# Kernel tuning notes

Hardware: AMD Instinct MI355X
Metric: run time of the kernel (lower is better)

Reference implementation:

```python
import jax, jax.numpy as jnp
import numpy as np

NUM_HEADS = 16
KEY_DIM = 64
EPS = 1e-6


def setup_inputs() -> dict:
    key = jax.random.key(0)
    k0, k1, k2, k3, k4 = jax.random.split(key, 5)
    B, S, E = 4, 4096, NUM_HEADS * KEY_DIM
    scale = 1.0 / np.sqrt(KEY_DIM)
    return {
        "query": jax.random.normal(k0, (B, S, E), dtype=jnp.float32),
        "Wq": jax.random.normal(k1, (NUM_HEADS, KEY_DIM, KEY_DIM), dtype=jnp.float32) * scale,
        "Wk": jax.random.normal(k2, (NUM_HEADS, KEY_DIM, KEY_DIM), dtype=jnp.float32) * scale,
        "Wv": jax.random.normal(k3, (NUM_HEADS, KEY_DIM, KEY_DIM), dtype=jnp.float32) * scale,
        "Wo": jax.random.normal(k4, (E, E), dtype=jnp.float32) * (1.0 / np.sqrt(E)),
    }


def reference(query, Wq, Wk, Wv, Wo):
    # Self-attention: key = value = query (per call() defaults).
    B, S, E = query.shape
    H, D = NUM_HEADS, KEY_DIM
    # split_heads: (B, S, E) -> (B, H, S, D)
    x = jnp.transpose(query.reshape(B, S, H, D), (0, 2, 1, 3))
    # Per-head linear projections (all heads batched in one einsum each).
    q = jnp.einsum("bhsd,hde->bhse", x, Wq)
    k = jnp.einsum("bhsd,hde->bhse", x, Wk)
    v = jnp.einsum("bhsd,hde->bhse", x, Wv)
    # Kernel feature map phi(x) = elu(x) + 1 (strictly positive).
    phi_q = jax.nn.elu(q) + 1.0
    phi_k = jax.nn.elu(k) + 1.0
    # Linear (non-causal) attention: O(S*D^2) instead of O(S^2*D).
    kv = jnp.einsum("bhsd,bhse->bhde", phi_k, v)        # (B,H,D,D)
    k_sum = jnp.sum(phi_k, axis=2)                       # (B,H,D)
    z = jnp.einsum("bhsd,bhd->bhs", phi_q, k_sum)        # (B,H,S)
    ctx = jnp.einsum("bhsd,bhde->bhse", phi_q, kv) / (z[..., None] + EPS)
    # combine_heads: (B,H,S,D) -> (B,S,E), then output projection (no bias).
    combined = jnp.transpose(ctx, (0, 2, 1, 3)).reshape(B, S, H * D)
    return combined @ Wo
```

## Files before the change

### kernel.cpp

```cpp
#include <hip/hip_runtime.h>
#include <stdint.h>

#define S_LEN 4096
#define NHEADS 16
#define DHEAD 64
#define EMB 1024
#define NBATCH 4
#define NBH (NBATCH * NHEADS)

typedef unsigned short u16t;
typedef __attribute__((ext_vector_type(8))) short short8;
typedef __attribute__((ext_vector_type(4))) float f32x4;

__device__ __forceinline__ u16t f2bf(float f) {
  unsigned int x = __float_as_uint(f);
  x += 0x7fffu + ((x >> 16) & 1u);
  return (u16t)(x >> 16);
}
__device__ __forceinline__ unsigned int pack2(float a, float b) {
  return (unsigned int)f2bf(a) | ((unsigned int)f2bf(b) << 16);
}
__device__ __forceinline__ float bf2f(u16t u) { return __uint_as_float(((unsigned int)u) << 16); }
__device__ __forceinline__ float phifn(float v) { return v > 0.f ? v + 1.f : __expf(v); }

__device__ __forceinline__ void stage_x_bf16(const float* __restrict__ xg,
                                             u16t* __restrict__ xs, int t) {
#pragma unroll
  for (int i = 0; i < 8; ++i) {
    int fi = i * 256 + t;
    int r = fi >> 4, c4 = fi & 15;
    float4 v = *(const float4*)(xg + (size_t)r * EMB + c4 * 4);
    uint2 p;
    p.x = pack2(v.x, v.y);
    p.y = pack2(v.z, v.w);
    *(uint2*)(&xs[r * 72 + c4 * 4]) = p;
  }
}

__device__ __forceinline__ void stage_w8k(const u16t* __restrict__ wg,
                                          u16t* __restrict__ lds, int t) {
#pragma unroll
  for (int c = 0; c < 2; ++c) {
    const u16t* src = wg + (size_t)(c * 256 + t) * 8;
    char* dst = (char*)lds + c * 4096 + ((t >> 6) << 10);
    __builtin_amdgcn_global_load_lds((const __attribute__((address_space(1))) unsigned int*)src,
                                     (__attribute__((address_space(3))) unsigned int*)dst,
                                     16, 0, 0);
  }
}

__global__ __launch_bounds__(256) void la_prep(const float* __restrict__ Wq,
                                               const float* __restrict__ Wk,
                                               const float* __restrict__ Wv,
                                               u16t* __restrict__ WqT,
                                               u16t* __restrict__ WkT,
                                               u16t* __restrict__ WvT) {
  __shared__ float tmp[64][65];
  int blk = blockIdx.x;
  int mat = blk >> 4, h = blk & 15;
  const float* src = (mat == 0 ? Wq : (mat == 1 ? Wk : Wv)) + (size_t)h * 4096;
  u16t* dst = (mat == 0 ? WqT : (mat == 1 ? WkT : WvT)) + (size_t)h * 4096;
  int t = threadIdx.x;
#pragma unroll
  for (int p = 0; p < 16; ++p) {
    int i = p * 256 + t;
    tmp[i >> 6][i & 63] = src[i];
  }
  __syncthreads();
#pragma unroll
  for (int p = 0; p < 16; ++p) {
    int i = p * 256 + t;
    int e = i >> 6, r = i & 63, o = r >> 3, j = r & 7;
    dst[i] = f2bf(tmp[((o ^ (e & 7)) << 3) + j][e]);
  }
}

__global__ __launch_bounds__(256) void la_wot(const float* __restrict__ Wo,
                                              u16t* __restrict__ WoT) {
  __shared__ float t[64][65];
  int n0 = blockIdx.x * 64, k0 = blockIdx.y * 64;
  int tx = threadIdx.x, ty = threadIdx.y;
  for (int r = ty; r < 64; r += 4) t[r][tx] = Wo[(size_t)(k0 + r) * EMB + n0 + tx];
  __syncthreads();
  for (int r = ty; r < 64; r += 4)
    WoT[(size_t)(n0 + r) * EMB + k0 + tx] = f2bf(t[tx][r]);
}

__global__ __launch_bounds__(256) void la_kvq3(const float* __restrict__ q,
                                               const u16t* __restrict__ WqT,
                                               const u16t* __restrict__ WkT,
                                               const u16t* __restrict__ WvT,
                                               u16t* __restrict__ phiq,
                                               float* __restrict__ kvpart,
                                               float* __restrict__ kspart) {
  __shared__ u16t xs[128 * 72];
  __shared__ u16t wq[4096];
  __shared__ u16t wk[4096];
  __shared__ u16t wv[4096];
  __shared__ u16t pkT[64 * 136];
  __shared__ u16t vT[64 * 136];
  int blk = blockIdx.x;
  int bh = blk >> 3, tile = blk & 7;
  int b = bh >> 4, h = bh & 15;
  int s0 = tile << 9;
  int t = threadIdx.x;
  int wave = t >> 6, lane = t & 63, l16 = lane & 15, g = lane >> 4;

  stage_w8k(WqT + (size_t)h * 4096, wq, t);
  stage_w8k(WkT + (size_t)h * 4096, wk, t);
  stage_w8k(WvT + (size_t)h * 4096, wv, t);

  f32x4 kacc[4];
#pragma unroll
  for (int n = 0; n < 4; ++n) kacc[n] = 0.f;
  float ksacc = 0.f;

  for (int c = 0; c < 4; ++c) {
    if (c) __syncthreads();
    stage_x_bf16(q + ((size_t)b * S_LEN + s0 + c * 128) * EMB + h * 64, xs, t);
    __syncthreads();

    f32x4 aQ[2][4], aK[2][4], aV[2][4];
#pragma unroll
    for (int m = 0; m < 2; ++m)
#pragma unroll
      for (int n = 0; n < 4; ++n) { aQ[m][n] = 0.f; aK[m][n] = 0.f; aV[m][n] = 0.f; }
    short8 af[2][2];
#pragma unroll
    for (int m = 0; m < 2; ++m)
#pragma unroll
      for (int kk = 0; kk < 2; ++kk)
        af[m][kk] = *(const short8*)(&xs[(wave * 32 + m * 16 + l16) * 72 + kk * 32 + g * 8]);
#pragma unroll
    for (int n = 0; n < 4; ++n) {
      int e = n * 16 + l16;
#pragma unroll
      for (int kk = 0; kk < 2; ++kk) {
        int op = (kk * 4 + g) ^ (l16 & 7);
        short8 bQ = *(const short8*)(&wq[e * 64 + op * 8]);
        short8 bK = *(const short8*)(&wk[e * 64 + op * 8]);
        short8 bV = *(const short8*)(&wv[e * 64 + op * 8]);
#pragma unroll
        for (int m = 0; m < 2; ++m) {
          aQ[m][n] = __builtin_amdgcn_mfma_f32_16x16x32_bf16(af[m][kk], bQ, aQ[m][n], 0, 0, 0);
          aK[m][n] = __builtin_amdgcn_mfma_f32_16x16x32_bf16(af[m][kk], bK, aK[m][n], 0, 0, 0);
          aV[m][n] = __builtin_amdgcn_mfma_f32_16x16x32_bf16(af[m][kk], bV, aV[m][n], 0, 0, 0);
        }
      }
    }
    __syncthreads();

#pragma unroll
    for (int m = 0; m < 2; ++m)
#pragma unroll
      for (int n = 0; n < 4; ++n) {
        int e = n * 16 + l16;
#pragma unroll
        for (int j = 0; j < 4; ++j) {
          int s = wave * 32 + m * 16 + g * 4 + j;
          xs[s * 72 + e] = f2bf(phifn(aQ[m][n][j]));
          pkT[e * 136 + s] = f2bf(phifn(aK[m][n][j]));
          vT[e * 136 + s] = f2bf(aV[m][n][j]);
        }
      }
    __syncthreads();

#pragma unroll
    for (int i = 0; i < 4; ++i) {
      int slot = i * 256 + t;
      int r = slot >> 3, cc = (slot & 7) * 8;
      *(uint4*)(phiq + ((size_t)bh * S_LEN + s0 + c * 128 + r) * 64 + cc) =
          *(const uint4*)(&xs[r * 72 + cc]);
    }
#pragma unroll
    for (int ks = 0; ks < 4; ++ks) {
      short8 pa = *(const short8*)(&pkT[(wave * 16 + l16) * 136 + ks * 32 + g * 8]);
#pragma unroll
      for (int n = 0; n < 4; ++n) {
        short8 vb = *(const short8*)(&vT[(n * 16 + l16) * 136 + ks * 32 + g * 8]);
        kacc[n] = __builtin_amdgcn_mfma_f32_16x16x32_bf16(pa, vb, kacc[n], 0, 0, 0);
      }
    }
    if (t < 64) {
#pragma unroll 8
      for (int s = 0; s < 128; ++s) ksacc += bf2f(pkT[t * 136 + s]);
    }
  }

  float* kp = kvpart + (size_t)blk * 4096;
#pragma unroll
  for (int n = 0; n < 4; ++n)
#pragma unroll
    for (int j = 0; j < 4; ++j)
      kp[(wave * 16 + g * 4 + j) * 64 + n * 16 + l16] = kacc[n][j];
  if (t < 64) kspart[(size_t)blk * 64 + t] = ksacc;
}

__global__ __launch_bounds__(256) void la_red3(const float* __restrict__ kvpart,
                                               const float* __restrict__ kspart,
                                               const u16t* __restrict__ WoT,
                                               float* __restrict__ ksum_g,
                                               u16t* __restrict__ W2T) {
  __shared__ float kvs[64][65];
  __shared__ u16t aT[256 * 72];
  int bh = blockIdx.x;
  int b = bh >> 4, h = bh & 15;
  int t = threadIdx.x, wave = t >> 6, lane = t & 63, l16 = lane & 15, g = lane >> 4;

  float acc[16];
#pragma unroll
  for (int i = 0; i < 16; ++i) acc[i] = 0.f;
  for (int p = 0; p < 8; ++p) {
    const float* base = kvpart + ((size_t)bh * 8 + p) * 4096;
#pragma unroll
    for (int i = 0; i < 16; ++i) acc[i] += base[i * 256 + t];
  }
#pragma unroll
  for (int i = 0; i < 16; ++i) {
    int idx = i * 256 + t;
    kvs[idx >> 6][idx & 63] = acc[i];
  }
  if (t < 64) {
    float a = 0.f;
    for (int p = 0; p < 8; ++p) a += kspart[((size_t)bh * 8 + p) * 64 + t];
    ksum_g[(size_t)bh * 64 + t] = a;
  }
  __syncthreads();

  short8 kvbf[4][2];
#pragma unroll
  for (int n = 0; n < 4; ++n)
#pragma unroll
    for (int kk = 0; kk < 2; ++kk) {
      u16t* pp = (u16t*)&kvbf[n][kk];
#pragma unroll
      for (int i = 0; i < 8; ++i) pp[i] = f2bf(kvs[n * 16 + l16][kk * 32 + g * 8 + i]);
    }

  for (int ec = 0; ec < 4; ++ec) {
    if (ec) __syncthreads();
#pragma unroll
    for (int p = 0; p < 8; ++p) {
      int slot = p * 256 + t;
      int r = slot >> 3, cc = (slot & 7) * 8;
      *(uint4*)(&aT[r * 72 + cc]) =
          *(const uint4*)(WoT + (size_t)(ec * 256 + r) * 1024 + h * 64 + cc);
    }
    __syncthreads();
    f32x4 c2[4][4];
#pragma unroll
    for (int mi = 0; mi < 4; ++mi)
#pragma unroll
      for (int n = 0; n < 4; ++n) c2[mi][n] = 0.f;
#pragma unroll
    for (int kk = 0; kk < 2; ++kk)
#pragma unroll
      for (int mi = 0; mi < 4; ++mi) {
        short8 afr = *(const short8*)(&aT[(wave * 64 + mi * 16 + l16) * 72 + kk * 32 + g * 8]);
#pragma unroll
        for (int n = 0; n < 4; ++n)
          c2[mi][n] = __builtin_amdgcn_mfma_f32_16x16x32_bf16(afr, kvbf[n][kk], c2[mi][n], 0, 0, 0);
      }
    __syncthreads();
#pragma unroll
    for (int mi = 0; mi < 4; ++mi)
#pragma unroll
      for (int n = 0; n < 4; ++n)
#pragma unroll
        for (int j = 0; j < 4; ++j)
          aT[(wave * 64 + mi * 16 + g * 4 + j) * 72 + n * 16 + l16] = f2bf(c2[mi][n][j]);
    __syncthreads();
#pragma unroll
    for (int p = 0; p < 8; ++p) {
      int slot = p * 256 + t;
      int r = slot >> 3, cc = (slot & 7) * 8;
      *(uint4*)(W2T + ((size_t)b << 20) + (size_t)(ec * 256 + r) * 1024 + h * 64 + cc) =
          *(const uint4*)(&aT[r * 72 + cc]);
    }
  }
}

__global__ __launch_bounds__(256) void la_scale(const u16t* __restrict__ phiq,
                                                const float* __restrict__ ksum_g,
                                                u16t* __restrict__ phiq2) {
  __shared__ float ks[64];
  int blk = blockIdx.x;
  int bh = blk >> 4, sl = blk & 15;
  int b = bh >> 4, h = bh & 15;
  int s0 = sl * 256;
  int t = threadIdx.x;
  if (t < 64) ks[t] = ksum_g[(size_t)bh * 64 + t];
  __syncthreads();
  int c16 = t & 15, rg = t >> 4;
#pragma unroll 2
  for (int it = 0; it < 16; ++it) {
    int s = s0 + it * 16 + rg;
    uint2 u = *(const uint2*)(phiq + ((size_t)bh * S_LEN + s) * 64 + c16 * 4);
    float f0 = bf2f((u16t)(u.x & 0xffff)), f1 = bf2f((u16t)(u.x >> 16));
    float f2 = bf2f((u16t)(u.y & 0xffff)), f3 = bf2f((u16t)(u.y >> 16));
    float zp = f0 * ks[c16 * 4] + f1 * ks[c16 * 4 + 1] + f2 * ks[c16 * 4 + 2] + f3 * ks[c16 * 4 + 3];
    zp += __shfl_xor(zp, 1);
    zp += __shfl_xor(zp, 2);
    zp += __shfl_xor(zp, 4);
    zp += __shfl_xor(zp, 8);
    float inv = 1.f / (zp + 1e-6f);
    uint2 o;
    o.x = pack2(f0 * inv, f1 * inv);
    o.y = pack2(f2 * inv, f3 * inv);
    *(uint2*)(phiq2 + ((size_t)(b * S_LEN + s)) * EMB + h * 64 + c16 * 4) = o;
  }
}

__device__ __forceinline__ void stage_half(const u16t* __restrict__ gbase,
                                           u16t* __restrict__ lbuf,
                                           int half, int t) {
#pragma unroll
  for (int it = 0; it < 2; ++it) {
    int slot = it * 512 + t;
    int row = half * 128 + (slot >> 3);
    int oct = slot & 7;
    const u16t* src = gbase + (size_t)row * EMB + (((oct ^ (row & 7)) << 3));
    char* dst = (char*)lbuf + ((half * 128 + it * 64 + ((t >> 6) << 3)) << 7);
    __builtin_amdgcn_global_load_lds((const __attribute__((address_space(1))) unsigned int*)src,
                                     (__attribute__((address_space(3))) unsigned int*)dst,
                                     16, 0, 0);
  }
}

#define GFENCE asm volatile("" ::: "memory")

#define LOAD_A(QM)                                                              \
  _Pragma("unroll") for (int mi = 0; mi < 4; ++mi) _Pragma("unroll")            \
      for (int kk = 0; kk < 2; ++kk) {                                          \
    int rr = (QM) * 128 + wr2 * 64 + mi * 16 + l16;                             \
    afr[mi][kk] = *(const short8*)((const char*)Acur + rr * 128 +               \
                                   ((((kk << 2) | g) ^ (rr & 7)) << 4));        \
  }
#define LOAD_B(QN, DST)                                                         \
  _Pragma("unroll") for (int ni = 0; ni < 2; ++ni) _Pragma("unroll")            \
      for (int kk = 0; kk < 2; ++kk) {                                          \
    int rr = (QN) * 128 + wc2 * 32 + ni * 16 + l16;                             \
    DST[ni][kk] = *(const short8*)((const char*)Bcur + rr * 128 +               \
                                   ((((kk << 2) | g) ^ (rr & 7)) << 4));        \
  }
#define MFMA_Q(QM, QN, BF)                                                      \
  __builtin_amdgcn_s_setprio(1);                                                \
  _Pragma("unroll") for (int mi = 0; mi < 4; ++mi) _Pragma("unroll")            \
      for (int ni = 0; ni < 2; ++ni) {                                          \
    acc[QM][QN][mi][ni] = __builtin_amdgcn_mfma_f32_16x16x32_bf16(              \
        afr[mi][0], BF[ni][0], acc[QM][QN][mi][ni], 0, 0, 0);                   \
    acc[QM][QN][mi][ni] = __builtin_amdgcn_mfma_f32_16x16x32_bf16(              \
        afr[mi][1], BF[ni][1], acc[QM][QN][mi][ni], 0, 0, 0);                   \
  }                                                                             \
  __builtin_amdgcn_s_setprio(0);

#define BAR()                      \
  __builtin_amdgcn_s_barrier();    \
  GFENCE

__global__ __launch_bounds__(512, 2) void la_gemm9(const u16t* __restrict__ A,
                                                   const u16t* __restrict__ W2T,
                                                   float* __restrict__ C) {
  __shared__ u16t Al[2][16384];
  __shared__ u16t Bl[2][16384];
  int t = threadIdx.x;
  int bid = blockIdx.x;
  int swz = ((bid & 7) << 5) + (bid >> 3);
  int mt = swz >> 2, nt = swz & 3;
  const int M0 = mt * 256, N0 = nt * 256;
  const int b = mt >> 4;
  int wave = t >> 6, lane = t & 63;
  int l16 = lane & 15, g = lane >> 4;
  int wr2 = wave >> 2, wc2 = wave & 3;

  f32x4 acc[2][2][4][2];
#pragma unroll
  for (int qm = 0; qm < 2; ++qm)
#pragma unroll
    for (int qn = 0; qn < 2; ++qn)
#pragma unroll
      for (int mi = 0; mi < 4; ++mi)
#pragma unroll
        for (int ni = 0; ni < 2; ++ni) acc[qm][qn][mi][ni] = 0.f;

  const u16t* Asrc = A + (size_t)M0 * EMB;
  const u16t* Bsrc = W2T + ((size_t)b << 20) + (size_t)N0 * EMB;

  stage_half(Asrc, Al[0], 0, t);
  stage_half(Bsrc, Bl[0], 0, t);
  stage_half(Bsrc, Bl[0], 1, t);
  stage_half(Asrc, Al[0], 1, t);
  asm volatile("s_waitcnt vmcnt(4)" ::: "memory");
  BAR();

  short8 afr[4][2], bf0[2][2], bf1[2][2];

  for (int kt = 0; kt < 15; ++kt) {
    const u16t* Acur = Al[kt & 1];
    const u16t* Bcur = Bl[kt & 1];
    u16t* Anxt = Al[(kt + 1) & 1];
    u16t* Bnxt = Bl[(kt + 1) & 1];
    const u16t* An = Asrc + (kt + 1) * 64;
    const u16t* Bn = Bsrc + (kt + 1) * 64;
    LOAD_A(0);
    LOAD_B(0, bf0);
    stage_half(An, Anxt, 0, t);
    stage_half(Bn, Bnxt, 0, t);
    asm volatile("s_waitcnt vmcnt(6)" ::: "memory");
    BAR();
    MFMA_Q(0, 0, bf0);
    GFENCE;
    BAR();
    LOAD_B(1, bf1);
    stage_half(Bn, Bnxt, 1, t);
    asm volatile("s_waitcnt vmcnt(6)" ::: "memory");
    BAR();
    MFMA_Q(0, 1, bf1);
    GFENCE;
    BAR();
    LOAD_A(1);
    stage_half(An, Anxt, 1, t);
    BAR();
    MFMA_Q(1, 1, bf1);
    GFENCE;
    BAR();
    asm volatile("s_waitcnt vmcnt(4)" ::: "memory");
    BAR();
    MFMA_Q(1, 0, bf0);
    GFENCE;
    BAR();
  }
  {
    const u16t* Acur = Al[1];
    const u16t* Bcur = Bl[1];
    LOAD_A(0);
    LOAD_B(0, bf0);
    asm volatile("s_waitcnt vmcnt(2)" ::: "memory");
    BAR();
    MFMA_Q(0, 0, bf0);
    GFENCE;
    BAR();
    LOAD_B(1, bf1);
    asm volatile("s_waitcnt vmcnt(0)" ::: "memory");
    BAR();
    MFMA_Q(0, 1, bf1);
    GFENCE;
    BAR();
    LOAD_A(1);
    BAR();
    MFMA_Q(1, 1, bf1);
    GFENCE;
    BAR();
    BAR();
    MFMA_Q(1, 0, bf0);
    GFENCE;
  }

#pragma unroll
  for (int qm = 0; qm < 2; ++qm)
#pragma unroll
    for (int qn = 0; qn < 2; ++qn)
#pragma unroll
      for (int mi = 0; mi < 4; ++mi)
#pragma unroll
        for (int ni = 0; ni < 2; ++ni)
#pragma unroll
          for (int j = 0; j < 4; ++j) {
            int row = M0 + qm * 128 + wr2 * 64 + mi * 16 + g * 4 + j;
            int col = N0 + qn * 128 + wc2 * 32 + ni * 16 + l16;
            C[(size_t)row * EMB + col] = acc[qm][qn][mi][ni][j];
          }
}

extern "C" void kernel_launch(void* const* d_in, const int* in_sizes, int n_in,
                              void* d_out, int out_size, void* d_ws, size_t ws_size,
                              hipStream_t stream) {
  const float* query = (const float*)d_in[0];
  const float* Wq = (const float*)d_in[1];
  const float* Wk = (const float*)d_in[2];
  const float* Wv = (const float*)d_in[3];
  const float* Wo = (const float*)d_in[4];
  float* out = (float*)d_out;
  char* ws = (char*)d_ws;

  u16t* WoT     = (u16t*)(ws);
  u16t* WqT     = (u16t*)(ws + 2097152);
  u16t* WkT     = (u16t*)(ws + 2228224);
  u16t* WvT     = (u16t*)(ws + 2359296);
  u16t* phiq    = (u16t*)(ws + 2490368);
  float* kvpart = (float*)(ws + 36044800);
  float* kspart = (float*)(ws + 44433408);
  float* ksum_g = (float*)(ws + 44564480);
  u16t* W2T     = (u16t*)(ws + 44580864);
  u16t* phiq2   = (u16t*)(ws + 52969472);

  la_prep<<<48, 256, 0, stream>>>(Wq, Wk, Wv, WqT, WkT, WvT);
  la_wot<<<dim3(16, 16), dim3(64, 4), 0, stream>>>(Wo, WoT);
  la_kvq3<<<512, 256, 0, stream>>>(query, WqT, WkT, WvT, phiq, kvpart, kspart);
  la_red3<<<NBH, 256, 0, stream>>>(kvpart, kspart, WoT, ksum_g, W2T);
  la_scale<<<1024, 256, 0, stream>>>(phiq, ksum_g, phiq2);
  la_gemm9<<<256, 512, 0, stream>>>(phiq2, W2T, out);
}
```

Baseline: 114.8 us.

## Fuse 1/z normalization into output GEMM A-load and prefetch query in kvq

Replaces the la_scale pass, which wrote a rescaled bf16 copy of phi_q in (B,S,E) layout, with a small la_z kernel that computes only the per-row 1/z values. The output GEMM then reads phi_q directly from its per-head layout and applies the 1/z scale while loading A fragments. This removes a full write and re-read of the scaled activation. The kvq kernel also register-prefetches the next query chunk, uses packed uint2 stores for phi_k/v, and spreads the k_sum reduction across all threads. The trade-off is extra VALU work per A fragment in the GEMM inner loop (bf16 unpack, multiply, repack) and some additional register pressure.

Measured after the change: 150.4 us. 31.0% more time.

```diff
diff --git a/kernel.cpp b/kernel.cpp
--- a/kernel.cpp
+++ b/kernel.cpp
@@ -23,18 +23,14 @@
 __device__ __forceinline__ float bf2f(u16t u) { return __uint_as_float(((unsigned int)u) << 16); }
 __device__ __forceinline__ float phifn(float v) { return v > 0.f ? v + 1.f : __expf(v); }
 
-__device__ __forceinline__ void stage_x_bf16(const float* __restrict__ xg,
-                                             u16t* __restrict__ xs, int t) {
+__device__ __forceinline__ short8 scale8(short8 v, float s) {
+  short8 r;
 #pragma unroll
   for (int i = 0; i < 8; ++i) {
-    int fi = i * 256 + t;
-    int r = fi >> 4, c4 = fi & 15;
-    float4 v = *(const float4*)(xg + (size_t)r * EMB + c4 * 4);
-    uint2 p;
-    p.x = pack2(v.x, v.y);
-    p.y = pack2(v.z, v.w);
-    *(uint2*)(&xs[r * 72 + c4 * 4]) = p;
-  }
+    float f = __uint_as_float(((unsigned int)(u16t)v[i]) << 16) * s;
+    r[i] = (short)f2bf(f);
+  }
+  return r;
 }
 
 __device__ __forceinline__ void stage_w8k(const u16t* __restrict__ wg,
@@ -86,7 +82,7 @@
     WoT[(size_t)(n0 + r) * EMB + k0 + tx] = f2bf(t[tx][r]);
 }
 
-__global__ __launch_bounds__(256) void la_kvq3(const float* __restrict__ q,
+__global__ __launch_bounds__(256) void la_kvq4(const float* __restrict__ q,
                                                const u16t* __restrict__ WqT,
                                                const u16t* __restrict__ WkT,
                                                const u16t* __restrict__ WvT,
@@ -99,6 +95,7 @@
   __shared__ u16t wv[4096];
   __shared__ u16t pkT[64 * 136];
   __shared__ u16t vT[64 * 136];
+  __shared__ float ksp4[4][64];
   int blk = blockIdx.x;
   int bh = blk >> 3, tile = blk & 7;
   int b = bh >> 4, h = bh & 15;
@@ -110,14 +107,34 @@
   stage_w8k(WkT + (size_t)h * 4096, wk, t);
   stage_w8k(WvT + (size_t)h * 4096, wv, t);
 
+  const float* xg = q + ((size_t)b * S_LEN + s0) * EMB + h * 64;
+  int pr_r = t >> 4, pr_c4 = (t & 15) * 4;
+
+  float4 pre[8];
+#pragma unroll
+  for (int i = 0; i < 8; ++i)
+    pre[i] = *(const float4*)(xg + (size_t)(i * 16 + pr_r) * EMB + pr_c4);
+
   f32x4 kacc[4];
 #pragma unroll
   for (int n = 0; n < 4; ++n) kacc[n] = 0.f;
-  float ksacc = 0.f;
+  float ks_acc = 0.f;
+  int ks_e = t & 63, ks_q = t >> 6;
 
   for (int c = 0; c < 4; ++c) {
     if (c) __syncthreads();
-    stage_x_bf16(q + ((size_t)b * S_LEN + s0 + c * 128) * EMB + h * 64, xs, t);
+#pragma unroll
+    for (int i = 0; i < 8; ++i) {
+      uint2 p;
+      p.x = pack2(pre[i].x, pre[i].y);
+      p.y = pack2(pre[i].z, pre[i].w);
+      *(uint2*)(&xs[(i * 16 + pr_r) * 72 + pr_c4]) = p;
+    }
+    if (c < 3) {
+#pragma unroll
+      for (int i = 0; i < 8; ++i)
+        pre[i] = *(const float4*)(xg + (size_t)((c + 1) * 128 + i * 16 + pr_r) * EMB + pr_c4);
+    }
     __syncthreads();
 
     f32x4 aQ[2][4], aK[2][4], aV[2][4];
@@ -155,13 +172,16 @@
 #pragma unroll
       for (int n = 0; n < 4; ++n) {
         int e = n * 16 + l16;
-#pragma unroll
-        for (int j = 0; j < 4; ++j) {
-          int s = wave * 32 + m * 16 + g * 4 + j;
-          xs[s * 72 + e] = f2bf(phifn(aQ[m][n][j]));
-          pkT[e * 136 + s] = f2bf(phifn(aK[m][n][j]));
-          vT[e * 136 + s] = f2bf(aV[m][n][j]);
-        }
+        int sb = wave * 32 + m * 16 + g * 4;
+        uint2 pk2, vv2;
+        pk2.x = pack2(phifn(aK[m][n][0]), phifn(aK[m][n][1]));
+        pk2.y = pack2(phifn(aK[m][n][2]), phifn(aK[m][n][3]));
+        vv2.x = pack2(aV[m][n][0], aV[m][n][1]);
+        vv2.y = pack2(aV[m][n][2], aV[m][n][3]);
+        *(uint2*)(&pkT[e * 136 + sb]) = pk2;
+        *(uint2*)(&vT[e * 136 + sb]) = vv2;
+#pragma unroll
+        for (int j = 0; j < 4; ++j) xs[(sb + j) * 72 + e] = f2bf(phifn(aQ[m][n][j]));
       }
     __syncthreads();
 
@@ -181,9 +201,11 @@
         kacc[n] = __builtin_amdgcn_mfma_f32_16x16x32_bf16(pa, vb, kacc[n], 0, 0, 0);
       }
     }
-    if (t < 64) {
-#pragma unroll 8
-      for (int s = 0; s < 128; ++s) ksacc += bf2f(pkT[t * 136 + s]);
+#pragma unroll
+    for (int i = 0; i < 8; ++i) {
+      uint2 u = *(const uint2*)(&pkT[ks_e * 136 + ks_q * 32 + i * 4]);
+      ks_acc += bf2f((u16t)(u.x & 0xffff)) + bf2f((u16t)(u.x >> 16)) +
+                bf2f((u16t)(u.y & 0xffff)) + bf2f((u16t)(u.y >> 16));
     }
   }
 
@@ -193,7 +215,11 @@
 #pragma unroll
     for (int j = 0; j < 4; ++j)
       kp[(wave * 16 + g * 4 + j) * 64 + n * 16 + l16] = kacc[n][j];
-  if (t < 64) kspart[(size_t)blk * 64 + t] = ksacc;
+
+  ksp4[ks_q][ks_e] = ks_acc;
+  __syncthreads();
+  if (t < 64)
+    kspart[(size_t)blk * 64 + t] = ksp4[0][t] + ksp4[1][t] + ksp4[2][t] + ksp4[3][t];
 }
 
 __global__ __launch_bounds__(256) void la_red3(const float* __restrict__ kvpart,
@@ -280,35 +306,40 @@
   }
 }
 
-__global__ __launch_bounds__(256) void la_scale(const u16t* __restrict__ phiq,
-                                                const float* __restrict__ ksum_g,
-                                                u16t* __restrict__ phiq2) {
-  __shared__ float ks[64];
+__global__ __launch_bounds__(256) void la_z(const u16t* __restrict__ phiq,
+                                            const float* __restrict__ ksum_g,
+                                            float* __restrict__ invz_g) {
+  __shared__ float ksl[16 * 64];
+  __shared__ float zbuf[64][16];
   int blk = blockIdx.x;
-  int bh = blk >> 4, sl = blk & 15;
-  int b = bh >> 4, h = bh & 15;
-  int s0 = sl * 256;
+  int b = blk >> 6, s0 = (blk & 63) * 64;
   int t = threadIdx.x;
-  if (t < 64) ks[t] = ksum_g[(size_t)bh * 64 + t];
+  int h = t >> 4, sl = t & 15;
+  *(float4*)(&ksl[t * 4]) = *(const float4*)(ksum_g + (size_t)b * 1024 + t * 4);
   __syncthreads();
-  int c16 = t & 15, rg = t >> 4;
-#pragma unroll 2
-  for (int it = 0; it < 16; ++it) {
-    int s = s0 + it * 16 + rg;
-    uint2 u = *(const uint2*)(phiq + ((size_t)bh * S_LEN + s) * 64 + c16 * 4);
-    float f0 = bf2f((u16t)(u.x & 0xffff)), f1 = bf2f((u16t)(u.x >> 16));
-    float f2 = bf2f((u16t)(u.y & 0xffff)), f3 = bf2f((u16t)(u.y >> 16));
-    float zp = f0 * ks[c16 * 4] + f1 * ks[c16 * 4 + 1] + f2 * ks[c16 * 4 + 2] + f3 * ks[c16 * 4 + 3];
-    zp += __shfl_xor(zp, 1);
-    zp += __shfl_xor(zp, 2);
-    zp += __shfl_xor(zp, 4);
-    zp += __shfl_xor(zp, 8);
-    float inv = 1.f / (zp + 1e-6f);
-    uint2 o;
-    o.x = pack2(f0 * inv, f1 * inv);
-    o.y = pack2(f2 * inv, f3 * inv);
-    *(uint2*)(phiq2 + ((size_t)(b * S_LEN + s)) * EMB + h * 64 + c16 * 4) = o;
-  }
+#pragma unroll
+  for (int j = 0; j < 4; ++j) {
+    int s = s0 + j * 16 + sl;
+    const uint4* pr = (const uint4*)(phiq + ((size_t)(b * 16 + h) * S_LEN + s) * 64);
+    float z = 0.f;
+#pragma unroll
+    for (int u = 0; u < 8; ++u) {
+      uint4 w = pr[u];
+      const float* kd = &ksl[h * 64 + u * 8];
+      z = fmaf(bf2f((u16t)(w.x & 0xffff)), kd[0], z);
+      z = fmaf(bf2f((u16t)(w.x >> 16)), kd[1], z);
+      z = fmaf(bf2f((u16t)(w.y & 0xffff)), kd[2], z);
+      z = fmaf(bf2f((u16t)(w.y >> 16)), kd[3], z);
+      z = fmaf(bf2f((u16t)(w.z & 0xffff)), kd[4], z);
+      z = fmaf(bf2f((u16t)(w.z >> 16)), kd[5], z);
+      z = fmaf(bf2f((u16t)(w.w & 0xffff)), kd[6], z);
+      z = fmaf(bf2f((u16t)(w.w >> 16)), kd[7], z);
+    }
+    zbuf[j * 16 + sl][h] = 1.f / (z + 1e-6f);
+  }
+  __syncthreads();
+  int r = t >> 2, c4 = (t & 3) * 4;
+  *(float4*)(invz_g + ((size_t)b * S_LEN + s0 + r) * 16 + c4) = *(const float4*)(&zbuf[r][c4]);
 }
 
 __device__ __forceinline__ void stage_half(const u16t* __restrict__ gbase,
@@ -326,15 +357,33 @@
                                      16, 0, 0);
   }
 }
+__device__ __forceinline__ void stage_half_A(const u16t* __restrict__ gbase,
+                                             u16t* __restrict__ lbuf,
+                                             int half, int t) {
+#pragma unroll
+  for (int it = 0; it < 2; ++it) {
+    int slot = it * 512 + t;
+    int row = half * 128 + (slot >> 3);
+    int oct = slot & 7;
+    const u16t* src = gbase + (size_t)row * 64 + (((oct ^ (row & 7)) << 3));
+    char* dst = (char*)lbuf + ((half * 128 + it * 64 + ((t >> 6) << 3)) << 7);
+    __builtin_amdgcn_global_load_lds((const __attribute__((address_space(1))) unsigned int*)src,
+                                     (__attribute__((address_space(3))) unsigned int*)dst,
+                                     16, 0, 0);
+  }
+}
 
 #define GFENCE asm volatile("" ::: "memory")
 
 #define LOAD_A(QM)                                                              \
-  _Pragma("unroll") for (int mi = 0; mi < 4; ++mi) _Pragma("unroll")            \
-      for (int kk = 0; kk < 2; ++kk) {                                          \
+  _Pragma("unroll") for (int mi = 0; mi < 4; ++mi) {                            \
     int rr = (QM) * 128 + wr2 * 64 + mi * 16 + l16;                             \
-    afr[mi][kk] = *(const short8*)((const char*)Acur + rr * 128 +               \
-                                   ((((kk << 2) | g) ^ (rr & 7)) << 4));        \
+    float zz = invzs[rr * 20 + kth];                                            \
+    _Pragma("unroll") for (int kk = 0; kk < 2; ++kk) {                          \
+      short8 raw = *(const short8*)((const char*)Acur + rr * 128 +              \
+                                    ((((kk << 2) | g) ^ (rr & 7)) << 4));       \
+      afr[mi][kk] = scale8(raw, zz);                                            \
+    }                                                                           \
   }
 #define LOAD_B(QN, DST)                                                         \
   _Pragma("unroll") for (int ni = 0; ni < 2; ++ni) _Pragma("unroll")            \
@@ -358,17 +407,20 @@
   __builtin_amdgcn_s_barrier();    \
   GFENCE
 
-__global__ __launch_bounds__(512, 2) void la_gemm9(const u16t* __restrict__ A,
-                                                   const u16t* __restrict__ W2T,
-                                                   float* __restrict__ C) {
+__global__ __launch_bounds__(512, 2) void la_gemm10(const u16t* __restrict__ phiq,
+                                                    const u16t* __restrict__ W2T,
+                                                    const float* __restrict__ invz_g,
+                                                    float* __restrict__ C) {
   __shared__ u16t Al[2][16384];
   __shared__ u16t Bl[2][16384];
+  __shared__ float invzs[256 * 20];
   int t = threadIdx.x;
   int bid = blockIdx.x;
   int swz = ((bid & 7) << 5) + (bid >> 3);
   int mt = swz >> 2, nt = swz & 3;
   const int M0 = mt * 256, N0 = nt * 256;
   const int b = mt >> 4;
+  const int moff = M0 & 4095;
   int wave = t >> 6, lane = t & 63;
   int l16 = lane & 15, g = lane >> 4;
   int wr2 = wave >> 2, wc2 = wave & 3;
@@ -383,28 +435,37 @@
 #pragma unroll
         for (int ni = 0; ni < 2; ++ni) acc[qm][qn][mi][ni] = 0.f;
 
-  const u16t* Asrc = A + (size_t)M0 * EMB;
   const u16t* Bsrc = W2T + ((size_t)b << 20) + (size_t)N0 * EMB;
-
-  stage_half(Asrc, Al[0], 0, t);
+#define ASRC(KT) (phiq + ((size_t)(b * 16 + (KT)) * S_LEN + moff) * 64)
+
+  const uint4* zsrc = (const uint4*)(invz_g + (size_t)M0 * 16);
+  uint4 zv0 = zsrc[t * 2], zv1 = zsrc[t * 2 + 1];
+  stage_half_A(ASRC(0), Al[0], 0, t);
   stage_half(Bsrc, Bl[0], 0, t);
   stage_half(Bsrc, Bl[0], 1, t);
-  stage_half(Asrc, Al[0], 1, t);
+  stage_half_A(ASRC(0), Al[0], 1, t);
+  asm volatile("s_waitcnt vmcnt(8)" ::: "memory");
+  {
+    int r = t >> 1, h8 = (t & 1) * 8;
+    *(float4*)(&invzs[r * 20 + h8]) = *(const float4*)&zv0;
+    *(float4*)(&invzs[r * 20 + h8 + 4]) = *(const float4*)&zv1;
+  }
   asm volatile("s_waitcnt vmcnt(4)" ::: "memory");
   BAR();
 
   short8 afr[4][2], bf0[2][2], bf1[2][2];
 
   for (int kt = 0; kt < 15; ++kt) {
+    const int kth = kt;
     const u16t* Acur = Al[kt & 1];
     const u16t* Bcur = Bl[kt & 1];
     u16t* Anxt = Al[(kt + 1) & 1];
     u16t* Bnxt = Bl[(kt + 1) & 1];
-    const u16t* An = Asrc + (kt + 1) * 64;
+    const u16t* An = ASRC(kt + 1);
     const u16t* Bn = Bsrc + (kt + 1) * 64;
     LOAD_A(0);
     LOAD_B(0, bf0);
-    stage_half(An, Anxt, 0, t);
+    stage_half_A(An, Anxt, 0, t);
     stage_half(Bn, Bnxt, 0, t);
     asm volatile("s_waitcnt vmcnt(6)" ::: "memory");
     BAR();
@@ -419,7 +480,7 @@
     GFENCE;
     BAR();
     LOAD_A(1);
-    stage_half(An, Anxt, 1, t);
+    stage_half_A(An, Anxt, 1, t);
     BAR();
     MFMA_Q(1, 1, bf1);
     GFENCE;
@@ -431,6 +492,7 @@
     BAR();
   }
   {
+    const int kth = 15;
     const u16t* Acur = Al[1];
     const u16t* Bcur = Bl[1];
     LOAD_A(0);
@@ -470,6 +532,7 @@
             int col = N0 + qn * 128 + wc2 * 32 + ni * 16 + l16;
             C[(size_t)row * EMB + col] = acc[qm][qn][mi][ni][j];
           }
+#undef ASRC
 }
 
 extern "C" void kernel_launch(void* const* d_in, const int* in_sizes, int n_in,
@@ -492,12 +555,12 @@
   float* kspart = (float*)(ws + 44433408);
   float* ksum_g = (float*)(ws + 44564480);
   u16t* W2T     = (u16t*)(ws + 44580864);
-  u16t* phiq2   = (u16t*)(ws + 52969472);
+  float* invz   = (float*)(ws + 52969472);
 
   la_prep<<<48, 256, 0, stream>>>(Wq, Wk, Wv, WqT, WkT, WvT);
   la_wot<<<dim3(16, 16), dim3(64, 4), 0, stream>>>(Wo, WoT);
-  la_kvq3<<<512, 256, 0, stream>>>(query, WqT, WkT, WvT, phiq, kvpart, kspart);
+  la_kvq4<<<512, 256, 0, stream>>>(query, WqT, WkT, WvT, phiq, kvpart, kspart);
   la_red3<<<NBH, 256, 0, stream>>>(kvpart, kspart, WoT, ksum_g, W2T);
-  la_scale<<<1024, 256, 0, stream>>>(phiq, ksum_g, phiq2);
-  la_gemm9<<<256, 512, 0, stream>>>(phiq2, W2T, out);
-}
+  la_z<<<256, 256, 0, stream>>>(phiq, ksum_g, invz);
+  la_gemm10<<<256, 512, 0, stream>>>(phiq, W2T, invz, out);
+}
```

## Prefetch next query chunk into registers and parallelize key-sum reduction in kvq kernel

Applied to the files above, without the earlier changes.

The projection kernel now loads the next 128-row query chunk into registers while the current chunk is being processed, so global load latency overlaps with MFMA work. The phi(k) and v stores to the transposed LDS tiles are packed into 64-bit writes instead of scalar 16-bit writes. The per-block key-sum reduction is spread across all 256 threads with vectorized LDS reads and combined through a small shared buffer, replacing a serial 128-step loop run by one wave. Holding the prefetched chunk adds 32 registers per thread, which may lower occupancy.

Result: faster. 112.1 us (-2.4%).

```diff
diff --git a/kernel.cpp b/kernel.cpp
--- a/kernel.cpp
+++ b/kernel.cpp
@@ -22,20 +22,6 @@
 }
 __device__ __forceinline__ float bf2f(u16t u) { return __uint_as_float(((unsigned int)u) << 16); }
 __device__ __forceinline__ float phifn(float v) { return v > 0.f ? v + 1.f : __expf(v); }
-
-__device__ __forceinline__ void stage_x_bf16(const float* __restrict__ xg,
-                                             u16t* __restrict__ xs, int t) {
-#pragma unroll
-  for (int i = 0; i < 8; ++i) {
-    int fi = i * 256 + t;
-    int r = fi >> 4, c4 = fi & 15;
-    float4 v = *(const float4*)(xg + (size_t)r * EMB + c4 * 4);
-    uint2 p;
-    p.x = pack2(v.x, v.y);
-    p.y = pack2(v.z, v.w);
-    *(uint2*)(&xs[r * 72 + c4 * 4]) = p;
-  }
-}
 
 __device__ __forceinline__ void stage_w8k(const u16t* __restrict__ wg,
                                           u16t* __restrict__ lds, int t) {
@@ -86,7 +72,7 @@
     WoT[(size_t)(n0 + r) * EMB + k0 + tx] = f2bf(t[tx][r]);
 }
 
-__global__ __launch_bounds__(256) void la_kvq3(const float* __restrict__ q,
+__global__ __launch_bounds__(256) void la_kvq4(const float* __restrict__ q,
                                                const u16t* __restrict__ WqT,
                                                const u16t* __restrict__ WkT,
                                                const u16t* __restrict__ WvT,
@@ -99,6 +85,7 @@
   __shared__ u16t wv[4096];
   __shared__ u16t pkT[64 * 136];
   __shared__ u16t vT[64 * 136];
+  __shared__ float ksp4[4][64];
   int blk = blockIdx.x;
   int bh = blk >> 3, tile = blk & 7;
   int b = bh >> 4, h = bh & 15;
@@ -110,14 +97,34 @@
   stage_w8k(WkT + (size_t)h * 4096, wk, t);
   stage_w8k(WvT + (size_t)h * 4096, wv, t);
 
+  const float* xg = q + ((size_t)b * S_LEN + s0) * EMB + h * 64;
+  int pr_r = t >> 4, pr_c4 = (t & 15) * 4;
+
+  float4 pre[8];
+#pragma unroll
+  for (int i = 0; i < 8; ++i)
+    pre[i] = *(const float4*)(xg + (size_t)(i * 16 + pr_r) * EMB + pr_c4);
+
   f32x4 kacc[4];
 #pragma unroll
   for (int n = 0; n < 4; ++n) kacc[n] = 0.f;
-  float ksacc = 0.f;
+  float ks_acc = 0.f;
+  int ks_e = t & 63, ks_q = t >> 6;
 
   for (int c = 0; c < 4; ++c) {
     if (c) __syncthreads();
-    stage_x_bf16(q + ((size_t)b * S_LEN + s0 + c * 128) * EMB + h * 64, xs, t);
+#pragma unroll
+    for (int i = 0; i < 8; ++i) {
+      uint2 p;
+      p.x = pack2(pre[i].x, pre[i].y);
+      p.y = pack2(pre[i].z, pre[i].w);
+      *(uint2*)(&xs[(i * 16 + pr_r) * 72 + pr_c4]) = p;
+    }
+    if (c < 3) {
+#pragma unroll
+      for (int i = 0; i < 8; ++i)
+        pre[i] = *(const float4*)(xg + (size_t)((c + 1) * 128 + i * 16 + pr_r) * EMB + pr_c4);
+    }
     __syncthreads();
 
     f32x4 aQ[2][4], aK[2][4], aV[2][4];
@@ -155,13 +162,16 @@
 #pragma unroll
       for (int n = 0; n < 4; ++n) {
         int e = n * 16 + l16;
-#pragma unroll
-        for (int j = 0; j < 4; ++j) {
-          int s = wave * 32 + m * 16 + g * 4 + j;
-          xs[s * 72 + e] = f2bf(phifn(aQ[m][n][j]));
-          pkT[e * 136 + s] = f2bf(phifn(aK[m][n][j]));
-          vT[e * 136 + s] = f2bf(aV[m][n][j]);
-        }
+        int sb = wave * 32 + m * 16 + g * 4;
+        uint2 pk2, vv2;
+        pk2.x = pack2(phifn(aK[m][n][0]), phifn(aK[m][n][1]));
+        pk2.y = pack2(phifn(aK[m][n][2]), phifn(aK[m][n][3]));
+        vv2.x = pack2(aV[m][n][0], aV[m][n][1]);
+        vv2.y = pack2(aV[m][n][2], aV[m][n][3]);
+        *(uint2*)(&pkT[e * 136 + sb]) = pk2;
+        *(uint2*)(&vT[e * 136 + sb]) = vv2;
+#pragma unroll
+        for (int j = 0; j < 4; ++j) xs[(sb + j) * 72 + e] = f2bf(phifn(aQ[m][n][j]));
       }
     __syncthreads();
 
@@ -181,9 +191,11 @@
         kacc[n] = __builtin_amdgcn_mfma_f32_16x16x32_bf16(pa, vb, kacc[n], 0, 0, 0);
       }
     }
-    if (t < 64) {
-#pragma unroll 8
-      for (int s = 0; s < 128; ++s) ksacc += bf2f(pkT[t * 136 + s]);
+#pragma unroll
+    for (int i = 0; i < 8; ++i) {
+      uint2 u = *(const uint2*)(&pkT[ks_e * 136 + ks_q * 32 + i * 4]);
+      ks_acc += bf2f((u16t)(u.x & 0xffff)) + bf2f((u16t)(u.x >> 16)) +
+                bf2f((u16t)(u.y & 0xffff)) + bf2f((u16t)(u.y >> 16));
     }
   }
 
@@ -193,7 +205,11 @@
 #pragma unroll
     for (int j = 0; j < 4; ++j)
       kp[(wave * 16 + g * 4 + j) * 64 + n * 16 + l16] = kacc[n][j];
-  if (t < 64) kspart[(size_t)blk * 64 + t] = ksacc;
+
+  ksp4[ks_q][ks_e] = ks_acc;
+  __syncthreads();
+  if (t < 64)
+    kspart[(size_t)blk * 64 + t] = ksp4[0][t] + ksp4[1][t] + ksp4[2][t] + ksp4[3][t];
 }
 
 __global__ __launch_bounds__(256) void la_red3(const float* __restrict__ kvpart,
@@ -496,7 +512,7 @@
 
   la_prep<<<48, 256, 0, stream>>>(Wq, Wk, Wv, WqT, WkT, WvT);
   la_wot<<<dim3(16, 16), dim3(64, 4), 0, stream>>>(Wo, WoT);
-  la_kvq3<<<512, 256, 0, stream>>>(query, WqT, WkT, WvT, phiq, kvpart, kspart);
+  la_kvq4<<<512, 256, 0, stream>>>(query, WqT, WkT, WvT, phiq, kvpart, kspart);
   la_red3<<<NBH, 256, 0, stream>>>(kvpart, kspart, WoT, ksum_g, W2T);
   la_scale<<<1024, 256, 0, stream>>>(phiq, ksum_g, phiq2);
   la_gemm9<<<256, 512, 0, stream>>>(phiq2, W2T, out);
```
